# Optimization experiments

Hardware: AMD Instinct MI355X
Metric: run time of the kernel (lower is better)

The kernel has to match this reference:

```python
import jax, jax.numpy as jnp
import numpy as np

N, IN, HID, OUT, HEADS = 50000, 128, 128, 16, 4
EL, EG = 800000, 200000
NEG_SLOPE = 0.2


def setup_inputs() -> dict:
    key = jax.random.key(0)
    ks = jax.random.split(key, 24)
    def gn(k, shape, fan_in):
        return (jax.random.normal(k, shape, jnp.float32) / np.sqrt(fan_in)).astype(jnp.float32)
    inp = {}
    inp['x'] = jax.random.normal(ks[0], (N, IN), jnp.float32)
    inp['local_edge_index'] = jax.random.randint(ks[1], (2, EL), 0, N, jnp.int64 if jax.config.jax_enable_x64 else jnp.int32)
    inp['global_edge_index'] = jax.random.randint(ks[2], (2, EG), 0, N, jnp.int64 if jax.config.jax_enable_x64 else jnp.int32)
    # local_processor: Linear(IN, HID)
    inp['W1'] = gn(ks[3], (IN, HID), IN); inp['b1'] = jnp.zeros((HID,), jnp.float32)
    # GCNConv(HID, HID): weight + bias
    inp['Wg'] = gn(ks[4], (HID, HID), HID); inp['bg'] = jnp.zeros((HID,), jnp.float32)
    # GATConv(HID, HID, heads=4, concat=False): lin to HEADS*HID, att vectors, bias of size HID
    inp['Wa'] = gn(ks[5], (HID, HEADS * HID), HID)
    inp['att_src'] = gn(ks[6], (HEADS, HID), HID)
    inp['att_dst'] = gn(ks[7], (HEADS, HID), HID)
    inp['ba'] = jnp.zeros((HID,), jnp.float32)
    # hierarchical_pool: Linear(2*HID, HID)
    inp['Wp'] = gn(ks[8], (2 * HID, HID), 2 * HID); inp['bp'] = jnp.zeros((HID,), jnp.float32)
    # classifier: Linear(HID, HID//2) -> ReLU -> Linear(HID//2, OUT)
    inp['Wc1'] = gn(ks[9], (HID, HID // 2), HID); inp['bc1'] = jnp.zeros((HID // 2,), jnp.float32)
    inp['Wc2'] = gn(ks[10], (HID // 2, OUT), HID // 2); inp['bc2'] = jnp.zeros((OUT,), jnp.float32)
    # uncertainty_head: Linear(HID, OUT)
    inp['Wu'] = gn(ks[11], (HID, OUT), HID); inp['bu'] = jnp.zeros((OUT,), jnp.float32)
    return inp


def _add_self_loops(ei, n):
    loop = jnp.arange(n, dtype=ei.dtype)
    return jnp.concatenate([ei[0], loop]), jnp.concatenate([ei[1], loop])


def gcn_conv(x, ei, W, b):
    n = x.shape[0]
    xw = x @ W                                        # [N, HID]
    src, dst = _add_self_loops(ei, n)
    deg = jax.ops.segment_sum(jnp.ones_like(dst, dtype=xw.dtype), dst, num_segments=n)
    dinv = jax.lax.rsqrt(jnp.maximum(deg, 1e-12))     # deg >= 1 thanks to self-loops
    norm = dinv[src] * dinv[dst]                      # [E+N]
    msg = xw[src] * norm[:, None]                     # gather + scale
    return jax.ops.segment_sum(msg, dst, num_segments=n) + b


def gat_conv(x, ei, W, att_src, att_dst, b):
    n = x.shape[0]
    h, c = att_src.shape
    xw = (x @ W).reshape(n, h, c)                     # [N, H, C]
    a_s = jnp.einsum('nhc,hc->nh', xw, att_src)       # [N, H]
    a_d = jnp.einsum('nhc,hc->nh', xw, att_dst)
    src, dst = _add_self_loops(ei, n)
    e = jax.nn.leaky_relu(a_s[src] + a_d[dst], NEG_SLOPE)   # [E+N, H]
    emax = jax.ops.segment_max(e, dst, num_segments=n)      # stable edge-softmax per dst
    ee = jnp.exp(e - emax[dst])
    denom = jax.ops.segment_sum(ee, dst, num_segments=n)
    alpha = ee / (denom[dst] + 1e-16)                        # [E+N, H]
    out = jax.ops.segment_sum(xw[src] * alpha[:, :, None], dst, num_segments=n)  # [N,H,C]
    return out.mean(axis=1) + b                              # concat=False -> head mean


def reference(x, local_edge_index, global_edge_index, W1, b1, Wg, bg, Wa, att_src, att_dst, ba, Wp, bp, Wc1, bc1, Wc2, bc2, Wu, bu):
    x_local = jax.nn.relu(x @ W1 + b1)                       # dropout is identity in eval
    x_lg = jax.nn.relu(gcn_conv(x_local, local_edge_index, Wg, bg))
    x_gg = jax.nn.relu(gat_conv(x_local, global_edge_index, Wa, att_src, att_dst, ba))
    x_comb = jnp.concatenate([x_lg, x_gg], axis=1)           # [N, 2*HID]
    x_pooled = jax.nn.relu(x_comb @ Wp + bp)
    x_final = x_pooled.mean(axis=0, keepdims=True)           # batch=None path
    prediction = jax.nn.relu(x_final @ Wc1 + bc1) @ Wc2 + bc2
    uncertainty = jax.nn.sigmoid(x_final @ Wu + bu)
    return prediction, uncertainty
```

## Files before the change

kernel.cpp:

```cpp
#include <hip/hip_runtime.h>
#include <hip/hip_bf16.h>

#define N_NODES 50000
#define F_IN 128
#define HID 128
#define N_OUT 16
#define HEADS 4
#define EL 800000
#define EG 200000
#define NEG_SLOPE 0.2f
#define NB 196
#define GB 391

typedef short bf16x8 __attribute__((ext_vector_type(8)));
typedef float f32x4 __attribute__((ext_vector_type(4)));
typedef float f32x2 __attribute__((ext_vector_type(2)));

static __device__ __forceinline__ float lrelu(float x) {
    return x > 0.f ? x : NEG_SLOPE * x;
}
static __device__ __forceinline__ unsigned short f2b(float f) {
    __hip_bfloat16 h = __float2bfloat16(f);
    return *reinterpret_cast<unsigned short*>(&h);
}
static __device__ __forceinline__ unsigned char f2fp8(float f) {
    unsigned pk = __builtin_amdgcn_cvt_pk_fp8_f32(f, f, 0, false);
    return (unsigned char)(pk & 0xFF);
}
static __device__ __forceinline__ f32x2 fp8x2_to_f32(unsigned u) {
    return __builtin_amdgcn_cvt_pk_f32_fp8((int)u, false);
}
static __device__ __forceinline__ float rdlane_f(float v, int l) {
    return __int_as_float(__builtin_amdgcn_readlane(__float_as_int(v), l));
}

__global__ __launch_bounds__(256) void conv_hist(
    const float* __restrict__ W1, unsigned short* __restrict__ W1t,
    const float* __restrict__ Wg, unsigned short* __restrict__ Wgt,
    const float* __restrict__ Wa, unsigned short* __restrict__ Wat,
    const float* __restrict__ Wp, unsigned short* __restrict__ Wpt,
    const int* __restrict__ ldst, const int* __restrict__ gdst, int* __restrict__ ghist)
{
    int b = blockIdx.x, t = threadIdx.x;
    if (b < 64) {
        int idx = b * 256 + t;
        int k = idx >> 7, n = idx & 127;
        W1t[n * 128 + k] = f2b(W1[idx]);
    } else if (b < 128) {
        int idx = (b - 64) * 256 + t;
        int k = idx >> 7, n = idx & 127;
        Wgt[n * 128 + k] = f2b(Wg[idx]);
    } else if (b < 384) {
        int idx = (b - 128) * 256 + t;
        int k = idx >> 9, n = idx & 511;
        Wat[(size_t)n * 128 + k] = f2b(Wa[idx]);
    } else if (b < 512) {
        int idx = (b - 384) * 256 + t;
        int k = idx >> 7, n = idx & 127;
        Wpt[(size_t)n * 256 + k] = f2b(Wp[idx]);
    } else {
        __shared__ int lh[NB];
        int blk = b - 512;
        bool loc = blk < 196;
        const int* dstp = loc ? ldst : gdst;
        int nE = loc ? EL : EG;
        int* gh = ghist + (loc ? 0 : NB);
        int start = (loc ? blk : blk - 196) * 4096;
        if (t < NB) lh[t] = 0;
        __syncthreads();
        #pragma unroll
        for (int i = 0; i < 16; i++) {
            int e = start + i * 256 + t;
            if (e < nE) atomicAdd(&lh[dstp[e] >> 8], 1);
        }
        __syncthreads();
        if (t < NB && lh[t]) atomicAdd(&gh[t], lh[t]);
    }
}
__global__ void bucket_scan(const int* __restrict__ ghist,
                            int* __restrict__ bbase, int* __restrict__ gcur)
{
    __shared__ int s[256];
    int g = blockIdx.x, t = threadIdx.x;
    int v = (t < NB) ? ghist[g * NB + t] : 0;
    s[t] = v;
    __syncthreads();
    for (int off = 1; off < 256; off <<= 1) {
        int u = (t >= off) ? s[t - off] : 0;
        __syncthreads();
        s[t] += u;
        __syncthreads();
    }
    if (t < NB) {
        bbase[g * (NB + 1) + t] = s[t] - v;
        gcur[g * NB + t] = s[t] - v;
    }
    if (t == NB - 1) bbase[g * (NB + 1) + NB] = s[t];
}
__global__ __launch_bounds__(256) void bucket_part(
    const int* __restrict__ lsrc, const int* __restrict__ ldst,
    const int* __restrict__ gsrc, const int* __restrict__ gdst,
    int* __restrict__ gcur, unsigned* __restrict__ ebuf_l, unsigned* __restrict__ ebuf_g)
{
    __shared__ int lhist[NB], lbase[NB];
    int blk = blockIdx.x, t = threadIdx.x;
    bool loc = blk < 196;
    const int* srcp = loc ? lsrc : gsrc;
    const int* dstp = loc ? ldst : gdst;
    int nE = loc ? EL : EG;
    unsigned* ebuf = loc ? ebuf_l : ebuf_g;
    int* cur = gcur + (loc ? 0 : NB);
    int start = (loc ? blk : blk - 196) * 4096;
    if (t < NB) lhist[t] = 0;
    __syncthreads();
    unsigned pk[16];
    #pragma unroll
    for (int i = 0; i < 16; i++) {
        int e = start + i * 256 + t;
        if (e < nE) {
            unsigned d = (unsigned)dstp[e];
            pk[i] = (d << 16) | (unsigned)srcp[e];
            atomicAdd(&lhist[d >> 8], 1);
        } else pk[i] = 0xFFFFFFFFu;
    }
    __syncthreads();
    if (t < NB) lbase[t] = atomicAdd(&cur[t], lhist[t]);
    __syncthreads();
    if (t < NB) lhist[t] = 0;
    __syncthreads();
    #pragma unroll
    for (int i = 0; i < 16; i++) {
        unsigned b = pk[i] >> 24;
        if (b < NB) {
            int r = atomicAdd(&lhist[b], 1);
            ebuf[lbase[b] + r] = pk[i];
        }
    }
}
__global__ __launch_bounds__(256) void bucket_csr(
    const unsigned* __restrict__ ebuf_l, const unsigned* __restrict__ ebuf_g,
    const int* __restrict__ bbase,
    int* __restrict__ offs_l, int* __restrict__ offs_g,
    unsigned short* __restrict__ csr_l, unsigned short* __restrict__ csr_g,
    float* __restrict__ dinv)
{
    __shared__ int cnt[256], s[256], cur[256];
    int blk = blockIdx.x, t = threadIdx.x;
    bool loc = blk < 196;
    int b = loc ? blk : blk - 196;
    const unsigned* ebuf = loc ? ebuf_l : ebuf_g;
    const int* bb = bbase + (loc ? 0 : NB + 1);
    int* offs = loc ? offs_l : offs_g;
    unsigned short* csr = loc ? csr_l : csr_g;
    int rs = bb[b], re = bb[b + 1];
    cnt[t] = 0;
    __syncthreads();
    for (int i = rs + t; i < re; i += 256) atomicAdd(&cnt[(ebuf[i] >> 16) & 255], 1);
    __syncthreads();
    int v = cnt[t];
    s[t] = v;
    __syncthreads();
    for (int off = 1; off < 256; off <<= 1) {
        int u = (t >= off) ? s[t - off] : 0;
        __syncthreads();
        s[t] += u;
        __syncthreads();
    }
    int excl = s[t] - v;
    int node = b * 256 + t;
    cur[t] = rs + excl;
    if (node < N_NODES) {
        offs[node] = rs + excl;
        if (loc) dinv[node] = rsqrtf((float)(v + 1));
    }
    if (blk == 0 && t == 0) offs_l[N_NODES] = EL;
    if (blk == 196 && t == 0) offs_g[N_NODES] = EG;
    __syncthreads();
    for (int i = rs + t; i < re; i += 256) {
        unsigned pk = ebuf[i];
        int r = atomicAdd(&cur[(pk >> 16) & 255], 1);
        csr[r] = (unsigned short)(pk & 0xFFFFu);
    }
}

__global__ __launch_bounds__(256) void gemm_x(
    const float* __restrict__ A, const unsigned short* __restrict__ Bt,
    const float* __restrict__ bias, unsigned short* __restrict__ out, int M)
{
    __shared__ unsigned short As[128 * 128];
    __shared__ unsigned short Bs[128 * 128];
    int tid = threadIdx.x;
    int lane = tid & 63, w = tid >> 6;
    int wr = w >> 1, wc = w & 1;
    int l16 = lane & 15, lhi = lane >> 4;
    int m0 = blockIdx.x * 128;
    f32x4 acc[4][4] = {};
    #pragma unroll
    for (int i = 0; i < 8; i++) {
        int u = tid + i * 256;
        int row = u >> 4, e0 = (u & 15) << 3;
        int sw = e0 ^ ((row & 7) << 3);
        int gr = m0 + row;
        unsigned short pb[8] = {};
        if (gr < M) {
            float4 a0 = *(const float4*)(A + (size_t)gr * 128 + e0);
            float4 a1 = *(const float4*)(A + (size_t)gr * 128 + e0 + 4);
            pb[0] = f2b(a0.x); pb[1] = f2b(a0.y); pb[2] = f2b(a0.z); pb[3] = f2b(a0.w);
            pb[4] = f2b(a1.x); pb[5] = f2b(a1.y); pb[6] = f2b(a1.z); pb[7] = f2b(a1.w);
        }
        *(bf16x8*)(As + row * 128 + sw) = *(bf16x8*)pb;
        bf16x8 vb = *(const bf16x8*)(Bt + (size_t)row * 128 + e0);
        *(bf16x8*)(Bs + row * 128 + sw) = vb;
    }
    __syncthreads();
    #pragma unroll
    for (int kk = 0; kk < 4; kk++) {
        int ke = kk * 32 + lhi * 8;
        bf16x8 af[4], bfr[4];
        #pragma unroll
        for (int m = 0; m < 4; m++) {
            int r = wr * 64 + m * 16 + l16;
            af[m] = *(const bf16x8*)(As + r * 128 + (ke ^ ((r & 7) << 3)));
        }
        #pragma unroll
        for (int n = 0; n < 4; n++) {
            int r = wc * 64 + n * 16 + l16;
            bfr[n] = *(const bf16x8*)(Bs + r * 128 + (ke ^ ((r & 7) << 3)));
        }
        #pragma unroll
        for (int m = 0; m < 4; m++)
            #pragma unroll
            for (int n = 0; n < 4; n++)
                acc[m][n] = __builtin_amdgcn_mfma_f32_16x16x32_bf16(af[m], bfr[n], acc[m][n], 0, 0, 0);
    }
    #pragma unroll
    for (int m = 0; m < 4; m++) {
        #pragma unroll
        for (int r = 0; r < 4; r++) {
            int row_g = m0 + wr * 64 + m * 16 + lhi * 4 + r;
            if (row_g >= M) continue;
            #pragma unroll
            for (int n = 0; n < 4; n++) {
                int col_g = wc * 64 + n * 16 + l16;
                float v = fmaxf(acc[m][n][r] + bias[col_g], 0.f);
                out[(size_t)row_g * 128 + col_g] = f2b(v);
            }
        }
    }
}

__global__ __launch_bounds__(256) void gemm_gw(
    const unsigned short* __restrict__ A, const unsigned short* __restrict__ Wgt,
    const unsigned short* __restrict__ Wat,
    unsigned char* __restrict__ xw_g8, unsigned char* __restrict__ xw_a8, int M,
    const float* __restrict__ atts, const float* __restrict__ attd,
    float* __restrict__ a_s, float* __restrict__ a_d,
    const float* __restrict__ dinv)
{
    __shared__ unsigned short As[128 * 128];
    __shared__ unsigned short Bs[128 * 128];
    __shared__ float sas[128], sad[128];
    int tid = threadIdx.x;
    int lane = tid & 63, w = tid >> 6;
    int wr = w >> 1, wc = w & 1;
    int l16 = lane & 15, lhi = lane >> 4;
    int m0 = blockIdx.x * 128;
    int hy = (int)blockIdx.y - 1;
    const unsigned short* Bt = (hy < 0) ? Wgt : (Wat + (size_t)hy * 128 * 128);
    f32x4 acc[4][4] = {};
    #pragma unroll
    for (int i = 0; i < 8; i++) {
        int u = tid + i * 256;
        int row = u >> 4, e0 = (u & 15) << 3;
        int sw = e0 ^ ((row & 7) << 3);
        bf16x8 va = {};
        int gr = m0 + row;
        if (gr < M) va = *(const bf16x8*)(A + (size_t)gr * 128 + e0);
        *(bf16x8*)(As + row * 128 + sw) = va;
        bf16x8 vb = *(const bf16x8*)(Bt + (size_t)row * 128 + e0);
        *(bf16x8*)(Bs + row * 128 + sw) = vb;
    }
    if (tid < 128) { sas[tid] = 0.f; sad[tid] = 0.f; }
    __syncthreads();
    #pragma unroll
    for (int kk = 0; kk < 4; kk++) {
        int ke = kk * 32 + lhi * 8;
        bf16x8 af[4], bfr[4];
        #pragma unroll
        for (int m = 0; m < 4; m++) {
            int r = wr * 64 + m * 16 + l16;
            af[m] = *(const bf16x8*)(As + r * 128 + (ke ^ ((r & 7) << 3)));
        }
        #pragma unroll
        for (int n = 0; n < 4; n++) {
            int r = wc * 64 + n * 16 + l16;
            bfr[n] = *(const bf16x8*)(Bs + r * 128 + (ke ^ ((r & 7) << 3)));
        }
        #pragma unroll
        for (int m = 0; m < 4; m++)
            #pragma unroll
            for (int n = 0; n < 4; n++)
                acc[m][n] = __builtin_amdgcn_mfma_f32_16x16x32_bf16(af[m], bfr[n], acc[m][n], 0, 0, 0);
    }
    if (hy < 0) {
        #pragma unroll
        for (int m = 0; m < 4; m++)
            #pragma unroll
            for (int r = 0; r < 4; r++) {
                int row_g = m0 + wr * 64 + m * 16 + lhi * 4 + r;
                if (row_g >= M) continue;
                float dv = dinv[row_g];
                #pragma unroll
                for (int n = 0; n < 4; n++) {
                    int col_g = wc * 64 + n * 16 + l16;
                    xw_g8[(size_t)row_g * 128 + col_g] = f2fp8(acc[m][n][r] * dv);
                }
            }
    } else {
        float ats[4], atd[4];
        #pragma unroll
        for (int n = 0; n < 4; n++) {
            int cl = wc * 64 + n * 16 + l16;
            ats[n] = atts[hy * 128 + cl];
            atd[n] = attd[hy * 128 + cl];
        }
        #pragma unroll
        for (int m = 0; m < 4; m++) {
            #pragma unroll
            for (int r = 0; r < 4; r++) {
                int row_l = wr * 64 + m * 16 + lhi * 4 + r;
                int row_g = m0 + row_l;
                float ps = 0.f, pd = 0.f;
                #pragma unroll
                for (int n = 0; n < 4; n++) {
                    float v = acc[m][n][r];
                    ps = fmaf(v, ats[n], ps);
                    pd = fmaf(v, atd[n], pd);
                    if (row_g < M) {
                        int col_g = hy * 128 + wc * 64 + n * 16 + l16;
                        xw_a8[(size_t)row_g * 512 + col_g] = f2fp8(v);
                    }
                }
                #pragma unroll
                for (int off = 1; off < 16; off <<= 1) {
                    ps += __shfl_xor(ps, off);
                    pd += __shfl_xor(pd, off);
                }
                if (l16 == 0) {
                    atomicAdd(&sas[row_l], ps);
                    atomicAdd(&sad[row_l], pd);
                }
            }
        }
        __syncthreads();
        if (tid < 128) {
            int row_g = m0 + tid;
            if (row_g < M) {
                a_s[(size_t)row_g * 4 + hy] = sas[tid];
                a_d[(size_t)row_g * 4 + hy] = sad[tid];
            }
        }
    }
}

__global__ __launch_bounds__(256) void fused_gather(
    const int* __restrict__ offs_l, const unsigned short* __restrict__ csr_l,
    const unsigned char* __restrict__ xw_g8, const float* __restrict__ dinv,
    const float* __restrict__ bg,
    const int* __restrict__ offs_g, const unsigned short* __restrict__ csr_g,
    const float* __restrict__ a_s, const float* __restrict__ a_d,
    const unsigned char* __restrict__ xw_a8, const float* __restrict__ ba,
    unsigned short* __restrict__ xcomb)
{
    int blk = blockIdx.x;
    int tid = threadIdx.x;
    int lane = tid & 63;
    int g = lane >> 4, q = lane & 15;
    if (blk < 12500) {
        int d = (blk * 256 + tid) >> 6;
        if (d >= N_NODES) return;
        int base = offs_l[d], end = offs_l[d + 1];
        unsigned goff = (unsigned)q * 8u;
        f32x2 a0 = {0.f, 0.f}, a1 = {0.f, 0.f}, a2 = {0.f, 0.f}, a3 = {0.f, 0.f};
        for (int i = base; i < end; ) {
            int chunk = min(64, end - i);
            int sv = (lane < chunk) ? (int)csr_l[i + lane] : 0;
            int nst = (chunk + 3) >> 2;
            for (int j = 0; j < nst; j++) {
                int e = j * 4 + g;
                int s = __shfl(sv, e);
                float mk = (e < chunk) ? 1.f : 0.f;
                f32x2 m2 = {mk, mk};
                uint2 v = *(const uint2*)(xw_g8 + (((unsigned)s) << 7) + goff);
                a0 += __builtin_amdgcn_cvt_pk_f32_fp8((int)v.x, false) * m2;
                a1 += __builtin_amdgcn_cvt_pk_f32_fp8((int)v.x, true) * m2;
                a2 += __builtin_amdgcn_cvt_pk_f32_fp8((int)v.y, false) * m2;
                a3 += __builtin_amdgcn_cvt_pk_f32_fp8((int)v.y, true) * m2;
            }
            i += chunk;
        }
        float av[8] = {a0[0], a0[1], a1[0], a1[1], a2[0], a2[1], a3[0], a3[1]};
        #pragma unroll
        for (int k = 0; k < 8; k++) {
            av[k] += __shfl_xor(av[k], 16);
            av[k] += __shfl_xor(av[k], 32);
        }
        if (g == 0) {
            float dd = dinv[d];
            uint2 sv2 = *(const uint2*)(xw_g8 + (((unsigned)d) << 7) + goff);
            f32x2 s0 = fp8x2_to_f32(sv2.x & 0xFFFFu);
            f32x2 s1 = __builtin_amdgcn_cvt_pk_f32_fp8((int)sv2.x, true);
            f32x2 s2 = fp8x2_to_f32(sv2.y & 0xFFFFu);
            f32x2 s3 = __builtin_amdgcn_cvt_pk_f32_fp8((int)sv2.y, true);
            float sf[8] = {s0[0], s0[1], s1[0], s1[1], s2[0], s2[1], s3[0], s3[1]};
            float4 b0 = *(const float4*)(bg + q * 8);
            float4 b1 = *(const float4*)(bg + q * 8 + 4);
            float bb[8] = {b0.x, b0.y, b0.z, b0.w, b1.x, b1.y, b1.z, b1.w};
            unsigned o[4];
            #pragma unroll
            for (int k = 0; k < 4; k++) {
                float v0 = fmaxf(dd * (av[2 * k] + sf[2 * k]) + bb[2 * k], 0.f);
                float v1 = fmaxf(dd * (av[2 * k + 1] + sf[2 * k + 1]) + bb[2 * k + 1], 0.f);
                o[k] = (unsigned)f2b(v0) | ((unsigned)f2b(v1) << 16);
            }
            *(uint4*)(xcomb + (size_t)d * 256 + q * 8) = make_uint4(o[0], o[1], o[2], o[3]);
        }
    } else {
        int d = ((blk - 12500) * 256 + tid) >> 6;
        if (d >= N_NODES) return;
        int base = offs_g[d], end = offs_g[d + 1];
        int deg = end - base;
        if (deg <= 16) {
            float ad_g = a_d[(size_t)d * 4 + g];
            float es = lrelu(a_s[(size_t)d * 4 + g] + ad_g);
            int sv = (q < deg) ? (int)csr_g[base + q] : 0;
            float asg = a_s[(size_t)sv * 4 + g];
            float e = (q < deg) ? lrelu(asg + ad_g) : -1e30f;
            float m = e;
            m = fmaxf(m, __shfl_xor(m, 1));
            m = fmaxf(m, __shfl_xor(m, 2));
            m = fmaxf(m, __shfl_xor(m, 4));
            m = fmaxf(m, __shfl_xor(m, 8));
            m = fmaxf(m, es);
            float wgt = (q < deg) ? __expf(e - m) : 0.f;
            float den = wgt;
            den += __shfl_xor(den, 1);
            den += __shfl_xor(den, 2);
            den += __shfl_xor(den, 4);
            den += __shfl_xor(den, 8);
            float se = __expf(es - m);
            den += se;
            float rinv = 0.25f / (den + 1e-16f);
            float wf = wgt * rinv;
            float selfw = se * rinv;
            unsigned goff = (unsigned)(g * 128 + q * 8);
            int b48 = lane & 48;
            f32x2 a0 = {0.f, 0.f}, a1 = {0.f, 0.f}, a2 = {0.f, 0.f}, a3 = {0.f, 0.f};
            int j = 0;
            for (; j + 2 <= deg; j += 2) {
                int sA = __builtin_amdgcn_readlane(sv, j);
                int sB = __builtin_amdgcn_readlane(sv, j + 1);
                float alA = __shfl(wf, b48 + j);
                float alB = __shfl(wf, b48 + j + 1);
                uint2 vA = *(const uint2*)(xw_a8 + (((unsigned)sA) << 9) + goff);
                uint2 vB = *(const uint2*)(xw_a8 + (((unsigned)sB) << 9) + goff);
                f32x2 mA = {alA, alA}, mB = {alB, alB};
                a0 += __builtin_amdgcn_cvt_pk_f32_fp8((int)vA.x, false) * mA;
                a1 += __builtin_amdgcn_cvt_pk_f32_fp8((int)vA.x, true) * mA;
                a2 += __builtin_amdgcn_cvt_pk_f32_fp8((int)vA.y, false) * mA;
                a3 += __builtin_amdgcn_cvt_pk_f32_fp8((int)vA.y, true) * mA;
                a0 += __builtin_amdgcn_cvt_pk_f32_fp8((int)vB.x, false) * mB;
                a1 += __builtin_amdgcn_cvt_pk_f32_fp8((int)vB.x, true) * mB;
                a2 += __builtin_amdgcn_cvt_pk_f32_fp8((int)vB.y, false) * mB;
                a3 += __builtin_amdgcn_cvt_pk_f32_fp8((int)vB.y, true) * mB;
            }
            if (j < deg) {
                int sA = __builtin_amdgcn_readlane(sv, j);
                float alA = __shfl(wf, b48 + j);
                uint2 vA = *(const uint2*)(xw_a8 + (((unsigned)sA) << 9) + goff);
                f32x2 mA = {alA, alA};
                a0 += __builtin_amdgcn_cvt_pk_f32_fp8((int)vA.x, false) * mA;
                a1 += __builtin_amdgcn_cvt_pk_f32_fp8((int)vA.x, true) * mA;
                a2 += __builtin_amdgcn_cvt_pk_f32_fp8((int)vA.y, false) * mA;
                a3 += __builtin_amdgcn_cvt_pk_f32_fp8((int)vA.y, true) * mA;
            }
            {
                uint2 v = *(const uint2*)(xw_a8 + (((unsigned)d) << 9) + goff);
                f32x2 ms = {selfw, selfw};
                a0 += __builtin_amdgcn_cvt_pk_f32_fp8((int)v.x, false) * ms;
                a1 += __builtin_amdgcn_cvt_pk_f32_fp8((int)v.x, true) * ms;
                a2 += __builtin_amdgcn_cvt_pk_f32_fp8((int)v.y, false) * ms;
                a3 += __builtin_amdgcn_cvt_pk_f32_fp8((int)v.y, true) * ms;
            }
            float av[8] = {a0[0], a0[1], a1[0], a1[1], a2[0], a2[1], a3[0], a3[1]};
            #pragma unroll
            for (int k = 0; k < 8; k++) {
                av[k] += __shfl_xor(av[k], 16);
                av[k] += __shfl_xor(av[k], 32);
            }
            if (g == 0) {
                float4 b0 = *(const float4*)(ba + q * 8);
                float4 b1 = *(const float4*)(ba + q * 8 + 4);
                float bb[8] = {b0.x, b0.y, b0.z, b0.w, b1.x, b1.y, b1.z, b1.w};
                unsigned o[4];
                #pragma unroll
                for (int k = 0; k < 4; k++) {
                    float v0 = fmaxf(av[2 * k] + bb[2 * k], 0.f);
                    float v1 = fmaxf(av[2 * k + 1] + bb[2 * k + 1], 0.f);
                    o[k] = (unsigned)f2b(v0) | ((unsigned)f2b(v1) << 16);
                }
                *(uint4*)(xcomb + (size_t)d * 256 + 128 + q * 8) = make_uint4(o[0], o[1], o[2], o[3]);
            }
            return;
        }
        float4 ad4 = *(const float4*)(a_d + (size_t)d * 4);
        float4 asd = *(const float4*)(a_s + (size_t)d * 4);
        float es0 = lrelu(asd.x + ad4.x), es1 = lrelu(asd.y + ad4.y);
        float es2 = lrelu(asd.z + ad4.z), es3 = lrelu(asd.w + ad4.w);
        if (deg <= 64) {
            int sv = 0;
            float e0 = -1e30f, e1 = -1e30f, e2 = -1e30f, e3 = -1e30f;
            if (lane < deg) {
                sv = csr_g[base + lane];
                float4 s4 = *(const float4*)(a_s + (size_t)sv * 4);
                e0 = lrelu(s4.x + ad4.x); e1 = lrelu(s4.y + ad4.y);
                e2 = lrelu(s4.z + ad4.z); e3 = lrelu(s4.w + ad4.w);
            }
            float m0 = e0, m1 = e1, m2 = e2, m3 = e3;
            #pragma unroll
            for (int off = 1; off < 64; off <<= 1) {
                m0 = fmaxf(m0, __shfl_xor(m0, off));
                m1 = fmaxf(m1, __shfl_xor(m1, off));
                m2 = fmaxf(m2, __shfl_xor(m2, off));
                m3 = fmaxf(m3, __shfl_xor(m3, off));
            }
            m0 = fmaxf(m0, es0); m1 = fmaxf(m1, es1);
            m2 = fmaxf(m2, es2); m3 = fmaxf(m3, es3);
            float w0 = (lane < deg) ? __expf(e0 - m0) : 0.f;
            float w1 = (lane < deg) ? __expf(e1 - m1) : 0.f;
            float w2 = (lane < deg) ? __expf(e2 - m2) : 0.f;
            float w3 = (lane < deg) ? __expf(e3 - m3) : 0.f;
            float d0 = w0, d1 = w1, d2 = w2, d3 = w3;
            #pragma unroll
            for (int off = 1; off < 64; off <<= 1) {
                d0 += __shfl_xor(d0, off); d1 += __shfl_xor(d1, off);
                d2 += __shfl_xor(d2, off); d3 += __shfl_xor(d3, off);
            }
            d0 += __expf(es0 - m0); d1 += __expf(es1 - m1);
            d2 += __expf(es2 - m2); d3 += __expf(es3 - m3);
            float r0 = 0.25f / (d0 + 1e-16f), r1 = 0.25f / (d1 + 1e-16f);
            float r2 = 0.25f / (d2 + 1e-16f), r3 = 0.25f / (d3 + 1e-16f);
            w0 *= r0; w1 *= r1; w2 *= r2; w3 *= r3;
            float wsel = (g == 0) ? w0 : (g == 1) ? w1 : (g == 2) ? w2 : w3;
            float selfw = (g == 0) ? __expf(es0 - m0) * r0 : (g == 1) ? __expf(es1 - m1) * r1
                        : (g == 2) ? __expf(es2 - m2) * r2 : __expf(es3 - m3) * r3;
            unsigned goff = (unsigned)(g * 128 + q * 8);
            f32x2 a0 = {0.f, 0.f}, a1 = {0.f, 0.f}, a2 = {0.f, 0.f}, a3 = {0.f, 0.f};
            for (int j = 0; j < deg; j++) {
                int s = __builtin_amdgcn_readlane(sv, j);
                float al = rdlane_f(wsel, j);
                uint2 v = *(const uint2*)(xw_a8 + (((unsigned)s) << 9) + goff);
                f32x2 mA = {al, al};
                a0 += __builtin_amdgcn_cvt_pk_f32_fp8((int)v.x, false) * mA;
                a1 += __builtin_amdgcn_cvt_pk_f32_fp8((int)v.x, true) * mA;
                a2 += __builtin_amdgcn_cvt_pk_f32_fp8((int)v.y, false) * mA;
                a3 += __builtin_amdgcn_cvt_pk_f32_fp8((int)v.y, true) * mA;
            }
            {
                uint2 v = *(const uint2*)(xw_a8 + (((unsigned)d) << 9) + goff);
                f32x2 ms = {selfw, selfw};
                a0 += __builtin_amdgcn_cvt_pk_f32_fp8((int)v.x, false) * ms;
                a1 += __builtin_amdgcn_cvt_pk_f32_fp8((int)v.x, true) * ms;
                a2 += __builtin_amdgcn_cvt_pk_f32_fp8((int)v.y, false) * ms;
                a3 += __builtin_amdgcn_cvt_pk_f32_fp8((int)v.y, true) * ms;
            }
            float av[8] = {a0[0], a0[1], a1[0], a1[1], a2[0], a2[1], a3[0], a3[1]};
            #pragma unroll
            for (int k = 0; k < 8; k++) {
                av[k] += __shfl_xor(av[k], 16);
                av[k] += __shfl_xor(av[k], 32);
            }
            if (g == 0) {
                float4 b0 = *(const float4*)(ba + q * 8);
                float4 b1 = *(const float4*)(ba + q * 8 + 4);
                float bb[8] = {b0.x, b0.y, b0.z, b0.w, b1.x, b1.y, b1.z, b1.w};
                unsigned o[4];
                #pragma unroll
                for (int k = 0; k < 4; k++) {
                    float v0 = fmaxf(av[2 * k] + bb[2 * k], 0.f);
                    float v1 = fmaxf(av[2 * k + 1] + bb[2 * k + 1], 0.f);
                    o[k] = (unsigned)f2b(v0) | ((unsigned)f2b(v1) << 16);
                }
                *(uint4*)(xcomb + (size_t)d * 256 + 128 + q * 8) = make_uint4(o[0], o[1], o[2], o[3]);
            }
        } else {
            int c2 = lane * 2;
            const unsigned short* xa = (const unsigned short*)xw_a8;
            float m0 = es0, m1 = es1, m2 = es2, m3 = es3;
            for (int i = base; i < end; i += 64) {
                int c = min(64, end - i);
                float t0 = -1e30f, t1 = -1e30f, t2 = -1e30f, t3 = -1e30f;
                if (lane < c) {
                    int s = csr_g[i + lane];
                    float4 s4 = *(const float4*)(a_s + (size_t)s * 4);
                    t0 = lrelu(s4.x + ad4.x); t1 = lrelu(s4.y + ad4.y);
                    t2 = lrelu(s4.z + ad4.z); t3 = lrelu(s4.w + ad4.w);
                }
                m0 = fmaxf(m0, t0); m1 = fmaxf(m1, t1);
                m2 = fmaxf(m2, t2); m3 = fmaxf(m3, t3);
            }
            #pragma unroll
            for (int off = 1; off < 64; off <<= 1) {
                m0 = fmaxf(m0, __shfl_xor(m0, off));
                m1 = fmaxf(m1, __shfl_xor(m1, off));
                m2 = fmaxf(m2, __shfl_xor(m2, off));
                m3 = fmaxf(m3, __shfl_xor(m3, off));
            }
            float d0 = 0.f, d1 = 0.f, d2 = 0.f, d3 = 0.f;
            for (int i = base; i < end; i += 64) {
                int c = min(64, end - i);
                if (lane < c) {
                    int s = csr_g[i + lane];
                    float4 s4 = *(const float4*)(a_s + (size_t)s * 4);
                    d0 += __expf(lrelu(s4.x + ad4.x) - m0);
                    d1 += __expf(lrelu(s4.y + ad4.y) - m1);
                    d2 += __expf(lrelu(s4.z + ad4.z) - m2);
                    d3 += __expf(lrelu(s4.w + ad4.w) - m3);
                }
            }
            #pragma unroll
            for (int off = 1; off < 64; off <<= 1) {
                d0 += __shfl_xor(d0, off); d1 += __shfl_xor(d1, off);
                d2 += __shfl_xor(d2, off); d3 += __shfl_xor(d3, off);
            }
            d0 += __expf(es0 - m0); d1 += __expf(es1 - m1);
            d2 += __expf(es2 - m2); d3 += __expf(es3 - m3);
            float r0 = 1.f / (d0 + 1e-16f), r1 = 1.f / (d1 + 1e-16f);
            float r2 = 1.f / (d2 + 1e-16f), r3 = 1.f / (d3 + 1e-16f);
            float ax = 0.f, ay = 0.f;
            for (int i = base; i < end; i += 64) {
                int c = min(64, end - i);
                int sv = 0;
                float w0 = 0.f, w1 = 0.f, w2 = 0.f, w3 = 0.f;
                if (lane < c) {
                    sv = csr_g[i + lane];
                    float4 s4 = *(const float4*)(a_s + (size_t)sv * 4);
                    w0 = __expf(lrelu(s4.x + ad4.x) - m0) * r0;
                    w1 = __expf(lrelu(s4.y + ad4.y) - m1) * r1;
                    w2 = __expf(lrelu(s4.z + ad4.z) - m2) * r2;
                    w3 = __expf(lrelu(s4.w + ad4.w) - m3) * r3;
                }
                for (int j = 0; j < c; j++) {
                    int s = __shfl(sv, j);
                    float a0 = __shfl(w0, j), a1 = __shfl(w1, j);
                    float a2 = __shfl(w2, j), a3 = __shfl(w3, j);
                    const unsigned short* row = xa + (size_t)s * 256 + lane;
                    f32x2 v0 = fp8x2_to_f32(row[0]);
                    f32x2 v1 = fp8x2_to_f32(row[64]);
                    f32x2 v2 = fp8x2_to_f32(row[128]);
                    f32x2 v3 = fp8x2_to_f32(row[192]);
                    ax = fmaf(v0[0], a0, ax); ay = fmaf(v0[1], a0, ay);
                    ax = fmaf(v1[0], a1, ax); ay = fmaf(v1[1], a1, ay);
                    ax = fmaf(v2[0], a2, ax); ay = fmaf(v2[1], a2, ay);
                    ax = fmaf(v3[0], a3, ax); ay = fmaf(v3[1], a3, ay);
                }
            }
            float s0 = __expf(es0 - m0) * r0, s1 = __expf(es1 - m1) * r1;
            float s2 = __expf(es2 - m2) * r2, s3 = __expf(es3 - m3) * r3;
            const unsigned short* row = xa + (size_t)d * 256 + lane;
            f32x2 v0 = fp8x2_to_f32(row[0]);
            f32x2 v1 = fp8x2_to_f32(row[64]);
            f32x2 v2 = fp8x2_to_f32(row[128]);
            f32x2 v3 = fp8x2_to_f32(row[192]);
            ax = fmaf(v0[0], s0, ax); ay = fmaf(v0[1], s0, ay);
            ax = fmaf(v1[0], s1, ax); ay = fmaf(v1[1], s1, ay);
            ax = fmaf(v2[0], s2, ax); ay = fmaf(v2[1], s2, ay);
            ax = fmaf(v3[0], s3, ax); ay = fmaf(v3[1], s3, ay);
            float ox = fmaxf(0.25f * ax + ba[c2], 0.f);
            float oy = fmaxf(0.25f * ay + ba[c2 + 1], 0.f);
            unsigned uo = (unsigned)f2b(ox) | ((unsigned)f2b(oy) << 16);
            *(unsigned*)(xcomb + (size_t)d * 256 + 128 + c2) = uo;
        }
    }
}

__global__ __launch_bounds__(256) void mfma_pool(
    const unsigned short* __restrict__ A, const unsigned short* __restrict__ Bt,
    const float* __restrict__ bp, float* __restrict__ sumvec, int M)
{
    __shared__ unsigned short As[128 * 128];
    __shared__ unsigned short Bs[128 * 128];
    __shared__ float red[128];
    int tid = threadIdx.x;
    int lane = tid & 63, w = tid >> 6;
    int wr = w >> 1, wc = w & 1;
    int l16 = lane & 15, lhi = lane >> 4;
    int m0 = blockIdx.x * 128;
    f32x4 acc[4][4] = {};
    for (int kb = 0; kb < 256; kb += 128) {
        if (kb) __syncthreads();
        #pragma unroll
        for (int i = 0; i < 8; i++) {
            int u = tid + i * 256;
            int row = u >> 4, e0 = (u & 15) << 3;
            int sw = e0 ^ ((row & 7) << 3);
            bf16x8 va = {};
            int gr = m0 + row;
            if (gr < M) va = *(const bf16x8*)(A + (size_t)gr * 256 + kb + e0);
            *(bf16x8*)(As + row * 128 + sw) = va;
            bf16x8 vb = *(const bf16x8*)(Bt + (size_t)row * 256 + kb + e0);
            *(bf16x8*)(Bs + row * 128 + sw) = vb;
        }
        __syncthreads();
        #pragma unroll
        for (int kk = 0; kk < 4; kk++) {
            int ke = kk * 32 + lhi * 8;
            bf16x8 af[4], bfr[4];
            #pragma unroll
            for (int m = 0; m < 4; m++) {
                int r = wr * 64 + m * 16 + l16;
                af[m] = *(const bf16x8*)(As + r * 128 + (ke ^ ((r & 7) << 3)));
            }
            #pragma unroll
            for (int n = 0; n < 4; n++) {
                int r = wc * 64 + n * 16 + l16;
                bfr[n] = *(const bf16x8*)(Bs + r * 128 + (ke ^ ((r & 7) << 3)));
            }
            #pragma unroll
            for (int m = 0; m < 4; m++)
                #pragma unroll
                for (int n = 0; n < 4; n++)
                    acc[m][n] = __builtin_amdgcn_mfma_f32_16x16x32_bf16(af[m], bfr[n], acc[m][n], 0, 0, 0);
        }
    }
    float bcol[4];
    #pragma unroll
    for (int n = 0; n < 4; n++) bcol[n] = bp[wc * 64 + n * 16 + l16];
    float colsum[4] = {0.f, 0.f, 0.f, 0.f};
    #pragma unroll
    for (int m = 0; m < 4; m++) {
        #pragma unroll
        for (int r = 0; r < 4; r++) {
            int row_g = m0 + wr * 64 + m * 16 + lhi * 4 + r;
            if (row_g < M) {
                #pragma unroll
                for (int n = 0; n < 4; n++)
                    colsum[n] += fmaxf(acc[m][n][r] + bcol[n], 0.f);
            }
        }
    }
    #pragma unroll
    for (int n = 0; n < 4; n++) {
        colsum[n] += __shfl_xor(colsum[n], 16);
        colsum[n] += __shfl_xor(colsum[n], 32);
    }
    if (tid < 128) red[tid] = 0.f;
    __syncthreads();
    if (lhi == 0) {
        #pragma unroll
        for (int n = 0; n < 4; n++)
            atomicAdd(&red[wc * 64 + n * 16 + l16], colsum[n]);
    }
    __syncthreads();
    if (tid < 128) atomicAdd(&sumvec[tid], red[tid]);
}

__global__ void final_head(const float* __restrict__ sumvec,
                           const float* __restrict__ Wc1, const float* __restrict__ bc1,
                           const float* __restrict__ Wc2, const float* __restrict__ bc2,
                           const float* __restrict__ Wu, const float* __restrict__ bu,
                           float* __restrict__ out)
{
    __shared__ float xf[128];
    __shared__ float h1[64];
    int t = threadIdx.x;
    xf[t] = sumvec[t] * (1.0f / N_NODES);
    __syncthreads();
    if (t < 64) {
        float s = bc1[t];
        for (int c = 0; c < 128; c++) s = fmaf(xf[c], Wc1[c * 64 + t], s);
        h1[t] = fmaxf(s, 0.f);
    }
    __syncthreads();
    if (t < 16) {
        float s = bc2[t];
        for (int j = 0; j < 64; j++) s = fmaf(h1[j], Wc2[j * 16 + t], s);
        out[t] = s;
        float u = bu[t];
        for (int c = 0; c < 128; c++) u = fmaf(xf[c], Wu[c * 16 + t], u);
        out[16 + t] = 1.0f / (1.0f + expf(-u));
    }
}

extern "C" void kernel_launch(void* const* d_in, const int* in_sizes, int n_in,
                              void* d_out, int out_size, void* d_ws, size_t ws_size,
                              hipStream_t stream) {
    const float* x    = (const float*)d_in[0];
    const int*   lei  = (const int*)d_in[1];
    const int*   gei  = (const int*)d_in[2];
    const float* W1   = (const float*)d_in[3];
    const float* b1   = (const float*)d_in[4];
    const float* Wg   = (const float*)d_in[5];
    const float* bg   = (const float*)d_in[6];
    const float* Wa   = (const float*)d_in[7];
    const float* atts = (const float*)d_in[8];
    const float* attd = (const float*)d_in[9];
    const float* ba   = (const float*)d_in[10];
    const float* Wp   = (const float*)d_in[11];
    const float* bp   = (const float*)d_in[12];
    const float* Wc1  = (const float*)d_in[13];
    const float* bc1  = (const float*)d_in[14];
    const float* Wc2  = (const float*)d_in[15];
    const float* bc2  = (const float*)d_in[16];
    const float* Wu   = (const float*)d_in[17];
    const float* bu   = (const float*)d_in[18];

    const int* lsrc = lei;
    const int* ldst = lei + EL;
    const int* gsrc = gei;
    const int* gdst = gei + EG;

    uintptr_t base = (uintptr_t)d_ws;
    auto alloc = [&](size_t bytes) { void* p = (void*)base; base += (bytes + 255) & ~(size_t)255; return p; };
    unsigned short* x_loc  = (unsigned short*)alloc((size_t)N_NODES * 128 * 2);
    unsigned char*  xw_g8  = (unsigned char*)alloc((size_t)N_NODES * 128);
    unsigned char*  xw_a8  = (unsigned char*)alloc((size_t)N_NODES * 512);
    unsigned short* xcomb  = (unsigned short*)alloc((size_t)N_NODES * 256 * 2);
    unsigned short* W1t    = (unsigned short*)alloc((size_t)128 * 128 * 2);
    unsigned short* Wgt    = (unsigned short*)alloc((size_t)128 * 128 * 2);
    unsigned short* Wat    = (unsigned short*)alloc((size_t)512 * 128 * 2);
    unsigned short* Wpt    = (unsigned short*)alloc((size_t)128 * 256 * 2);
    float* dinv       = (float*)alloc((size_t)N_NODES * 4);
    float* a_s        = (float*)alloc((size_t)N_NODES * 4 * 4);
    float* a_d        = (float*)alloc((size_t)N_NODES * 4 * 4);
    int*   ghist      = (int*)alloc((size_t)2 * NB * 4);
    int*   bbase      = (int*)alloc((size_t)2 * (NB + 1) * 4);
    int*   gcur       = (int*)alloc((size_t)2 * NB * 4);
    unsigned* ebuf_l  = (unsigned*)alloc((size_t)EL * 4);
    unsigned* ebuf_g  = (unsigned*)alloc((size_t)EG * 4);
    int*   offs_l     = (int*)alloc(((size_t)N_NODES + 1) * 4);
    int*   offs_g     = (int*)alloc(((size_t)N_NODES + 1) * 4);
    unsigned short* csr_l = (unsigned short*)alloc((size_t)EL * 2);
    unsigned short* csr_g = (unsigned short*)alloc((size_t)EG * 2);
    float* sumvec     = (float*)alloc(128 * 4);

    hipMemsetAsync(ghist, 0, (size_t)2 * NB * 4, stream);
    hipMemsetAsync(sumvec, 0, 128 * 4, stream);

    conv_hist<<<757, 256, 0, stream>>>(W1, W1t, Wg, Wgt, Wa, Wat, Wp, Wpt,
                                       ldst, gdst, ghist);
    bucket_scan<<<2, 256, 0, stream>>>(ghist, bbase, gcur);
    bucket_part<<<245, 256, 0, stream>>>(lsrc, ldst, gsrc, gdst, gcur, ebuf_l, ebuf_g);
    bucket_csr<<<392, 256, 0, stream>>>(ebuf_l, ebuf_g, bbase, offs_l, offs_g,
                                        csr_l, csr_g, dinv);

    gemm_x<<<GB, 256, 0, stream>>>(x, W1t, b1, x_loc, N_NODES);
    gemm_gw<<<dim3(GB, 5), 256, 0, stream>>>(x_loc, Wgt, Wat, xw_g8, xw_a8, N_NODES,
                                             atts, attd, a_s, a_d, dinv);

    fused_gather<<<25000, 256, 0, stream>>>(offs_l, csr_l, xw_g8, dinv, bg,
                                            offs_g, csr_g, a_s, a_d, xw_a8, ba, xcomb);

    mfma_pool<<<GB, 256, 0, stream>>>(xcomb, Wpt, bp, sumvec, N_NODES);
    final_head<<<1, 128, 0, stream>>>(sumvec, Wc1, bc1, Wc2, bc2, Wu, bu,
                                      (float*)d_out);
}
```

Before: 180.9 us.

## Fuse bucket scan into first GEMM, loop GEMM heads in-block, unroll gather

The tiny bucket-scan kernel is merged into the x@W1 GEMM launch as two extra blocks, removing one launch. The second GEMM now loops over the five weight matrices inside one block, so each A tile is loaded into shared memory once instead of five times across a 2D grid. The GCN gather loop is unrolled by two to keep two independent row loads in flight. The trade-off is fewer blocks in the second GEMM (391 instead of 1955), which lowers parallelism and adds per-iteration block syncs.

```diff
diff --git a/kernel.cpp b/kernel.cpp
--- a/kernel.cpp
+++ b/kernel.cpp
@@ -77,26 +77,93 @@
         if (t < NB && lh[t]) atomicAdd(&gh[t], lh[t]);
     }
 }
-__global__ void bucket_scan(const int* __restrict__ ghist,
-                            int* __restrict__ bbase, int* __restrict__ gcur)
+
+__global__ __launch_bounds__(256) void scan_gemmx(
+    const int* __restrict__ ghist, int* __restrict__ bbase, int* __restrict__ gcur,
+    const float* __restrict__ A, const unsigned short* __restrict__ Bt,
+    const float* __restrict__ bias, unsigned short* __restrict__ out, int M)
 {
-    __shared__ int s[256];
-    int g = blockIdx.x, t = threadIdx.x;
-    int v = (t < NB) ? ghist[g * NB + t] : 0;
-    s[t] = v;
-    __syncthreads();
-    for (int off = 1; off < 256; off <<= 1) {
-        int u = (t >= off) ? s[t - off] : 0;
+    __shared__ unsigned short As[128 * 128];
+    __shared__ unsigned short Bs[128 * 128];
+    int tid = threadIdx.x;
+    if (blockIdx.x < 2) {
+        int* s = (int*)As;
+        int g = blockIdx.x, t = tid;
+        int v = (t < NB) ? ghist[g * NB + t] : 0;
+        s[t] = v;
         __syncthreads();
-        s[t] += u;
-        __syncthreads();
-    }
-    if (t < NB) {
-        bbase[g * (NB + 1) + t] = s[t] - v;
-        gcur[g * NB + t] = s[t] - v;
-    }
-    if (t == NB - 1) bbase[g * (NB + 1) + NB] = s[t];
-}
+        for (int off = 1; off < 256; off <<= 1) {
+            int u = (t >= off) ? s[t - off] : 0;
+            __syncthreads();
+            s[t] += u;
+            __syncthreads();
+        }
+        if (t < NB) {
+            bbase[g * (NB + 1) + t] = s[t] - v;
+            gcur[g * NB + t] = s[t] - v;
+        }
+        if (t == NB - 1) bbase[g * (NB + 1) + NB] = s[t];
+        return;
+    }
+    int lane = tid & 63, w = tid >> 6;
+    int wr = w >> 1, wc = w & 1;
+    int l16 = lane & 15, lhi = lane >> 4;
+    int m0 = (blockIdx.x - 2) * 128;
+    f32x4 acc[4][4] = {};
+    #pragma unroll
+    for (int i = 0; i < 8; i++) {
+        int u = tid + i * 256;
+        int row = u >> 4, e0 = (u & 15) << 3;
+        int sw = e0 ^ ((row & 7) << 3);
+        int gr = m0 + row;
+        unsigned short pb[8] = {};
+        if (gr < M) {
+            float4 a0 = *(const float4*)(A + (size_t)gr * 128 + e0);
+            float4 a1 = *(const float4*)(A + (size_t)gr * 128 + e0 + 4);
+            pb[0] = f2b(a0.x); pb[1] = f2b(a0.y); pb[2] = f2b(a0.z); pb[3] = f2b(a0.w);
+            pb[4] = f2b(a1.x); pb[5] = f2b(a1.y); pb[6] = f2b(a1.z); pb[7] = f2b(a1.w);
+        }
+        *(bf16x8*)(As + row * 128 + sw) = *(bf16x8*)pb;
+        bf16x8 vb = *(const bf16x8*)(Bt + (size_t)row * 128 + e0);
+        *(bf16x8*)(Bs + row * 128 + sw) = vb;
+    }
+    __syncthreads();
+    #pragma unroll
+    for (int kk = 0; kk < 4; kk++) {
+        int ke = kk * 32 + lhi * 8;
+        bf16x8 af[4], bfr[4];
+        #pragma unroll
+        for (int m = 0; m < 4; m++) {
+            int r = wr * 64 + m * 16 + l16;
+            af[m] = *(const bf16x8*)(As + r * 128 + (ke ^ ((r & 7) << 3)));
+        }
+        #pragma unroll
+        for (int n = 0; n < 4; n++) {
+            int r = wc * 64 + n * 16 + l16;
+            bfr[n] = *(const bf16x8*)(Bs + r * 128 + (ke ^ ((r & 7) << 3)));
+        }
+        #pragma unroll
+        for (int m = 0; m < 4; m++)
+            #pragma unroll
+            for (int n = 0; n < 4; n++)
+                acc[m][n] = __builtin_amdgcn_mfma_f32_16x16x32_bf16(af[m], bfr[n], acc[m][n], 0, 0, 0);
+    }
+    #pragma unroll
+    for (int m = 0; m < 4; m++) {
+        #pragma unroll
+        for (int r = 0; r < 4; r++) {
+            int row_g = m0 + wr * 64 + m * 16 + lhi * 4 + r;
+            if (row_g >= M) continue;
+            #pragma unroll
+            for (int n = 0; n < 4; n++) {
+                int col_g = wc * 64 + n * 16 + l16;
+                float v = fmaxf(acc[m][n][r] + bias[col_g], 0.f);
+                out[(size_t)row_g * 128 + col_g] = f2b(v);
+            }
+        }
+    }
+}
+
 __global__ __launch_bounds__(256) void bucket_part(
     const int* __restrict__ lsrc, const int* __restrict__ ldst,
     const int* __restrict__ gsrc, const int* __restrict__ gdst,
@@ -183,73 +250,7 @@
     }
 }
 
-__global__ __launch_bounds__(256) void gemm_x(
-    const float* __restrict__ A, const unsigned short* __restrict__ Bt,
-    const float* __restrict__ bias, unsigned short* __restrict__ out, int M)
-{
-    __shared__ unsigned short As[128 * 128];
-    __shared__ unsigned short Bs[128 * 128];
-    int tid = threadIdx.x;
-    int lane = tid & 63, w = tid >> 6;
-    int wr = w >> 1, wc = w & 1;
-    int l16 = lane & 15, lhi = lane >> 4;
-    int m0 = blockIdx.x * 128;
-    f32x4 acc[4][4] = {};
-    #pragma unroll
-    for (int i = 0; i < 8; i++) {
-        int u = tid + i * 256;
-        int row = u >> 4, e0 = (u & 15) << 3;
-        int sw = e0 ^ ((row & 7) << 3);
-        int gr = m0 + row;
-        unsigned short pb[8] = {};
-        if (gr < M) {
-            float4 a0 = *(const float4*)(A + (size_t)gr * 128 + e0);
-            float4 a1 = *(const float4*)(A + (size_t)gr * 128 + e0 + 4);
-            pb[0] = f2b(a0.x); pb[1] = f2b(a0.y); pb[2] = f2b(a0.z); pb[3] = f2b(a0.w);
-            pb[4] = f2b(a1.x); pb[5] = f2b(a1.y); pb[6] = f2b(a1.z); pb[7] = f2b(a1.w);
-        }
-        *(bf16x8*)(As + row * 128 + sw) = *(bf16x8*)pb;
-        bf16x8 vb = *(const bf16x8*)(Bt + (size_t)row * 128 + e0);
-        *(bf16x8*)(Bs + row * 128 + sw) = vb;
-    }
-    __syncthreads();
-    #pragma unroll
-    for (int kk = 0; kk < 4; kk++) {
-        int ke = kk * 32 + lhi * 8;
-        bf16x8 af[4], bfr[4];
-        #pragma unroll
-        for (int m = 0; m < 4; m++) {
-            int r = wr * 64 + m * 16 + l16;
-            af[m] = *(const bf16x8*)(As + r * 128 + (ke ^ ((r & 7) << 3)));
-        }
-        #pragma unroll
-        for (int n = 0; n < 4; n++) {
-            int r = wc * 64 + n * 16 + l16;
-            bfr[n] = *(const bf16x8*)(Bs + r * 128 + (ke ^ ((r & 7) << 3)));
-        }
-        #pragma unroll
-        for (int m = 0; m < 4; m++)
-            #pragma unroll
-            for (int n = 0; n < 4; n++)
-                acc[m][n] = __builtin_amdgcn_mfma_f32_16x16x32_bf16(af[m], bfr[n], acc[m][n], 0, 0, 0);
-    }
-    #pragma unroll
-    for (int m = 0; m < 4; m++) {
-        #pragma unroll
-        for (int r = 0; r < 4; r++) {
-            int row_g = m0 + wr * 64 + m * 16 + lhi * 4 + r;
-            if (row_g >= M) continue;
-            #pragma unroll
-            for (int n = 0; n < 4; n++) {
-                int col_g = wc * 64 + n * 16 + l16;
-                float v = fmaxf(acc[m][n][r] + bias[col_g], 0.f);
-                out[(size_t)row_g * 128 + col_g] = f2b(v);
-            }
-        }
-    }
-}
-
-__global__ __launch_bounds__(256) void gemm_gw(
+__global__ __launch_bounds__(256) void gemm_gw5(
     const unsigned short* __restrict__ A, const unsigned short* __restrict__ Wgt,
     const unsigned short* __restrict__ Wat,
     unsigned char* __restrict__ xw_g8, unsigned char* __restrict__ xw_a8, int M,
@@ -265,9 +266,6 @@
     int wr = w >> 1, wc = w & 1;
     int l16 = lane & 15, lhi = lane >> 4;
     int m0 = blockIdx.x * 128;
-    int hy = (int)blockIdx.y - 1;
-    const unsigned short* Bt = (hy < 0) ? Wgt : (Wat + (size_t)hy * 128 * 128);
-    f32x4 acc[4][4] = {};
     #pragma unroll
     for (int i = 0; i < 8; i++) {
         int u = tid + i * 256;
@@ -277,87 +275,99 @@
         int gr = m0 + row;
         if (gr < M) va = *(const bf16x8*)(A + (size_t)gr * 128 + e0);
         *(bf16x8*)(As + row * 128 + sw) = va;
-        bf16x8 vb = *(const bf16x8*)(Bt + (size_t)row * 128 + e0);
-        *(bf16x8*)(Bs + row * 128 + sw) = vb;
-    }
-    if (tid < 128) { sas[tid] = 0.f; sad[tid] = 0.f; }
-    __syncthreads();
-    #pragma unroll
-    for (int kk = 0; kk < 4; kk++) {
-        int ke = kk * 32 + lhi * 8;
-        bf16x8 af[4], bfr[4];
-        #pragma unroll
-        for (int m = 0; m < 4; m++) {
-            int r = wr * 64 + m * 16 + l16;
-            af[m] = *(const bf16x8*)(As + r * 128 + (ke ^ ((r & 7) << 3)));
-        }
-        #pragma unroll
-        for (int n = 0; n < 4; n++) {
-            int r = wc * 64 + n * 16 + l16;
-            bfr[n] = *(const bf16x8*)(Bs + r * 128 + (ke ^ ((r & 7) << 3)));
-        }
-        #pragma unroll
-        for (int m = 0; m < 4; m++)
-            #pragma unroll
-            for (int n = 0; n < 4; n++)
-                acc[m][n] = __builtin_amdgcn_mfma_f32_16x16x32_bf16(af[m], bfr[n], acc[m][n], 0, 0, 0);
-    }
-    if (hy < 0) {
-        #pragma unroll
-        for (int m = 0; m < 4; m++)
-            #pragma unroll
-            for (int r = 0; r < 4; r++) {
-                int row_g = m0 + wr * 64 + m * 16 + lhi * 4 + r;
-                if (row_g >= M) continue;
-                float dv = dinv[row_g];
+    }
+    for (int p = 0; p < 5; p++) {
+        const unsigned short* Bt = (p == 0) ? Wgt : (Wat + (size_t)(p - 1) * 128 * 128);
+        __syncthreads();
+        #pragma unroll
+        for (int i = 0; i < 8; i++) {
+            int u = tid + i * 256;
+            int row = u >> 4, e0 = (u & 15) << 3;
+            int sw = e0 ^ ((row & 7) << 3);
+            bf16x8 vb = *(const bf16x8*)(Bt + (size_t)row * 128 + e0);
+            *(bf16x8*)(Bs + row * 128 + sw) = vb;
+        }
+        if (tid < 128) { sas[tid] = 0.f; sad[tid] = 0.f; }
+        __syncthreads();
+        f32x4 acc[4][4] = {};
+        #pragma unroll
+        for (int kk = 0; kk < 4; kk++) {
+            int ke = kk * 32 + lhi * 8;
+            bf16x8 af[4], bfr[4];
+            #pragma unroll
+            for (int m = 0; m < 4; m++) {
+                int r = wr * 64 + m * 16 + l16;
+                af[m] = *(const bf16x8*)(As + r * 128 + (ke ^ ((r & 7) << 3)));
+            }
+            #pragma unroll
+            for (int n = 0; n < 4; n++) {
+                int r = wc * 64 + n * 16 + l16;
+                bfr[n] = *(const bf16x8*)(Bs + r * 128 + (ke ^ ((r & 7) << 3)));
+            }
+            #pragma unroll
+            for (int m = 0; m < 4; m++)
                 #pragma unroll
-                for (int n = 0; n < 4; n++) {
-                    int col_g = wc * 64 + n * 16 + l16;
-                    xw_g8[(size_t)row_g * 128 + col_g] = f2fp8(acc[m][n][r] * dv);
-                }
-            }
-    } else {
-        float ats[4], atd[4];
-        #pragma unroll
-        for (int n = 0; n < 4; n++) {
-            int cl = wc * 64 + n * 16 + l16;
-            ats[n] = atts[hy * 128 + cl];
-            atd[n] = attd[hy * 128 + cl];
-        }
-        #pragma unroll
-        for (int m = 0; m < 4; m++) {
-            #pragma unroll
-            for (int r = 0; r < 4; r++) {
-                int row_l = wr * 64 + m * 16 + lhi * 4 + r;
-                int row_g = m0 + row_l;
-                float ps = 0.f, pd = 0.f;
+                for (int n = 0; n < 4; n++)
+                    acc[m][n] = __builtin_amdgcn_mfma_f32_16x16x32_bf16(af[m], bfr[n], acc[m][n], 0, 0, 0);
+        }
+        if (p == 0) {
+            #pragma unroll
+            for (int m = 0; m < 4; m++)
                 #pragma unroll
-                for (int n = 0; n < 4; n++) {
-                    float v = acc[m][n][r];
-                    ps = fmaf(v, ats[n], ps);
-                    pd = fmaf(v, atd[n], pd);
-                    if (row_g < M) {
-                        int col_g = hy * 128 + wc * 64 + n * 16 + l16;
-                        xw_a8[(size_t)row_g * 512 + col_g] = f2fp8(v);
+                for (int r = 0; r < 4; r++) {
+                    int row_g = m0 + wr * 64 + m * 16 + lhi * 4 + r;
+                    if (row_g >= M) continue;
+                    float dv = dinv[row_g];
+                    #pragma unroll
+                    for (int n = 0; n < 4; n++) {
+                        int col_g = wc * 64 + n * 16 + l16;
+                        xw_g8[(size_t)row_g * 128 + col_g] = f2fp8(acc[m][n][r] * dv);
                     }
                 }
+        } else {
+            int head = p - 1;
+            float ats[4], atd[4];
+            #pragma unroll
+            for (int n = 0; n < 4; n++) {
+                int cl = wc * 64 + n * 16 + l16;
+                ats[n] = atts[head * 128 + cl];
+                atd[n] = attd[head * 128 + cl];
+            }
+            #pragma unroll
+            for (int m = 0; m < 4; m++) {
                 #pragma unroll
-                for (int off = 1; off < 16; off <<= 1) {
-                    ps += __shfl_xor(ps, off);
-                    pd += __shfl_xor(pd, off);
+                for (int r = 0; r < 4; r++) {
+                    int row_l = wr * 64 + m * 16 + lhi * 4 + r;
+                    int row_g = m0 + row_l;
+                    float ps = 0.f, pd = 0.f;
+                    #pragma unroll
+                    for (int n = 0; n < 4; n++) {
+                        float v = acc[m][n][r];
+                        ps = fmaf(v, ats[n], ps);
+                        pd = fmaf(v, atd[n], pd);
+                        if (row_g < M) {
+                            int col_g = head * 128 + wc * 64 + n * 16 + l16;
+                            xw_a8[(size_t)row_g * 512 + col_g] = f2fp8(v);
+                        }
+                    }
+                    #pragma unroll
+                    for (int off = 1; off < 16; off <<= 1) {
+                        ps += __shfl_xor(ps, off);
+                        pd += __shfl_xor(pd, off);
+                    }
+                    if (l16 == 0) {
+                        atomicAdd(&sas[row_l], ps);
+                        atomicAdd(&sad[row_l], pd);
+                    }
                 }
-                if (l16 == 0) {
-                    atomicAdd(&sas[row_l], ps);
-                    atomicAdd(&sad[row_l], pd);
+            }
+            __syncthreads();
+            if (tid < 128) {
+                int row_g = m0 + tid;
+                if (row_g < M) {
+                    a_s[(size_t)row_g * 4 + head] = sas[tid];
+                    a_d[(size_t)row_g * 4 + head] = sad[tid];
                 }
-            }
-        }
-        __syncthreads();
-        if (tid < 128) {
-            int row_g = m0 + tid;
-            if (row_g < M) {
-                a_s[(size_t)row_g * 4 + hy] = sas[tid];
-                a_d[(size_t)row_g * 4 + hy] = sad[tid];
             }
         }
     }
@@ -386,7 +396,26 @@
             int chunk = min(64, end - i);
             int sv = (lane < chunk) ? (int)csr_l[i + lane] : 0;
             int nst = (chunk + 3) >> 2;
-            for (int j = 0; j < nst; j++) {
+            int j = 0;
+            for (; j + 2 <= nst; j += 2) {
+                int eA = j * 4 + g, eB = eA + 4;
+                int sA = __shfl(sv, eA);
+                int sB = __shfl(sv, eB);
+                float mkA = (eA < chunk) ? 1.f : 0.f;
+                float mkB = (eB < chunk) ? 1.f : 0.f;
+                uint2 vA = *(const uint2*)(xw_g8 + (((unsigned)sA) << 7) + goff);
+                uint2 vB = *(const uint2*)(xw_g8 + (((unsigned)sB) << 7) + goff);
+                f32x2 mA = {mkA, mkA}, mB = {mkB, mkB};
+                a0 += __builtin_amdgcn_cvt_pk_f32_fp8((int)vA.x, false) * mA;
+                a1 += __builtin_amdgcn_cvt_pk_f32_fp8((int)vA.x, true) * mA;
+                a2 += __builtin_amdgcn_cvt_pk_f32_fp8((int)vA.y, false) * mA;
+                a3 += __builtin_amdgcn_cvt_pk_f32_fp8((int)vA.y, true) * mA;
+                a0 += __builtin_amdgcn_cvt_pk_f32_fp8((int)vB.x, false) * mB;
+                a1 += __builtin_amdgcn_cvt_pk_f32_fp8((int)vB.x, true) * mB;
+                a2 += __builtin_amdgcn_cvt_pk_f32_fp8((int)vB.y, false) * mB;
+                a3 += __builtin_amdgcn_cvt_pk_f32_fp8((int)vB.y, true) * mB;
+            }
+            for (; j < nst; j++) {
                 int e = j * 4 + g;
                 int s = __shfl(sv, e);
                 float mk = (e < chunk) ? 1.f : 0.f;
@@ -849,18 +878,14 @@
 
     conv_hist<<<757, 256, 0, stream>>>(W1, W1t, Wg, Wgt, Wa, Wat, Wp, Wpt,
                                        ldst, gdst, ghist);
-    bucket_scan<<<2, 256, 0, stream>>>(ghist, bbase, gcur);
+    scan_gemmx<<<393, 256, 0, stream>>>(ghist, bbase, gcur, x, W1t, b1, x_loc, N_NODES);
     bucket_part<<<245, 256, 0, stream>>>(lsrc, ldst, gsrc, gdst, gcur, ebuf_l, ebuf_g);
     bucket_csr<<<392, 256, 0, stream>>>(ebuf_l, ebuf_g, bbase, offs_l, offs_g,
                                         csr_l, csr_g, dinv);
-
-    gemm_x<<<GB, 256, 0, stream>>>(x, W1t, b1, x_loc, N_NODES);
-    gemm_gw<<<dim3(GB, 5), 256, 0, stream>>>(x_loc, Wgt, Wat, xw_g8, xw_a8, N_NODES,
-                                             atts, attd, a_s, a_d, dinv);
-
+    gemm_gw5<<<GB, 256, 0, stream>>>(x_loc, Wgt, Wat, xw_g8, xw_a8, N_NODES,
+                                     atts, attd, a_s, a_d, dinv);
     fused_gather<<<25000, 256, 0, stream>>>(offs_l, csr_l, xw_g8, dinv, bg,
                                             offs_g, csr_g, a_s, a_d, xw_a8, ba, xcomb);
-
     mfma_pool<<<GB, 256, 0, stream>>>(xcomb, Wpt, bp, sumvec, N_NODES);
     final_head<<<1, 128, 0, stream>>>(sumvec, Wc1, bc1, Wc2, bc2, Wu, bu,
                                       (float*)d_out);
```

Measured after the change: 172.3 us. 1.05x faster.
